# Kernel tuning notes

Measured on AMD Instinct MI355X. Metric: run time of the kernel, lower is better.

The kernel has to match this reference:

```python
import jax, jax.numpy as jnp
import numpy as np

DIM = 1024
S_SIZE = 512
M_SIZE = 4096
L_SIZE = 8192
MERGE_THRESHOLD = 0.98
L_ALPHA = 0.1
K_PROMOTE = max(1, S_SIZE // 4)  # torch: min(len(candidates), max(1, s_size//4)); candidates >> s_size here


def _l2norm(x, axis=-1):
    # F.normalize(p=2) with eps clamp
    return x / jnp.maximum(jnp.linalg.norm(x, axis=axis, keepdims=True), 1e-12)


def _update(processed_tokens, s_memory, m_memory, l_memory, m_utility, l_utility, wq, bq, wk, bk, s_ptr):
    cand = processed_tokens.reshape(-1, DIM)
    # --- S tier: scatter top-k-norm candidates into ring buffer (vectorized; K<=S so slots distinct) ---
    norms = jnp.linalg.norm(cand, axis=1)
    _, top_idx = jax.lax.top_k(norms, K_PROMOTE)
    pos = (s_ptr + jnp.arange(K_PROMOTE)) % S_SIZE
    s_mem = s_memory.at[pos].set(cand[top_idx])
    s_ptr_new = (s_ptr + K_PROMOTE) % S_SIZE
    # --- promotion attention (1 head, only attn weights used): pick best short-term slot ---
    q = l_memory.mean(axis=0) @ wq.T + bq                      # [dim]
    kproj = s_mem @ wk.T + bk                                  # [S, dim]
    attn = jax.nn.softmax(kproj @ q / jnp.sqrt(jnp.asarray(DIM, cand.dtype)))
    best_s_idx = jnp.argmax(attn)
    candidate = s_mem[best_s_idx]                              # [dim]

    # --- M tier: promote / merge / replace ---
    def not_full(mm, mu):
        ridx = jnp.argmin(mu)
        return mm.at[ridx].set(candidate), mu.at[ridx].set(mu.mean() + 1e-5)

    def full(mm, mu):
        mm_norm = _l2norm(mm)
        sims = mm_norm @ _l2norm(candidate)                    # [M]
        msi = jnp.argmax(sims)
        sim_cand = sims[msi]

        def merge_with_candidate(mm, mu):
            merged = _l2norm((mm[msi] + candidate) / 2.0)
            return mm.at[msi].set(merged), mu.at[msi].set((mu[msi] + mu.mean()) / 2.0)

        def try_internal_merge(mm, mu):
            # most redundant pair: strict lower triangle of cosine sim matrix
            sim_mat = mm_norm @ mm_norm.T                      # [M, M]
            sim_mat = jnp.where(jnp.triu(jnp.ones((M_SIZE, M_SIZE), bool)), -1.0, sim_mat)
            flat = jnp.argmax(sim_mat)
            internal_sim = sim_mat.reshape(-1)[flat]
            idx1, idx2 = flat // M_SIZE, flat % M_SIZE

            def do_pair_merge(mm, mu):
                merged = _l2norm((mm[idx1] + mm[idx2]) / 2.0)
                mm2 = mm.at[idx1].set(merged).at[idx2].set(candidate)
                mu1 = mu.at[idx1].set((mu[idx1] + mu[idx2]) / 2.0)
                mu2 = mu1.at[idx2].set(mu1.mean() + 1e-5)      # torch recomputes mean after idx1 write
                return mm2, mu2

            def replace_weakest(mm, mu):
                li = jnp.argmin(mu)
                stronger = jnp.linalg.norm(candidate) > jnp.linalg.norm(mm[li])
                mm2 = jnp.where(stronger, mm.at[li].set(candidate), mm)
                mu2 = jnp.where(stronger, mu.at[li].set(mu.mean() + 1e-5), mu)
                return mm2, mu2

            return jax.lax.cond(internal_sim > MERGE_THRESHOLD, do_pair_merge, replace_weakest, mm, mu)

        return jax.lax.cond(sim_cand > MERGE_THRESHOLD, merge_with_candidate, try_internal_merge, mm, mu)

    is_m_full = ~jnp.any(m_utility == 0)
    m_mem, m_util = jax.lax.cond(is_m_full, full, not_full, m_memory, m_utility)
    # --- L tier: consolidate most-used M slot into least-used L slot ---
    mi = jnp.argmax(m_util)
    lj = jnp.argmin(l_utility)
    consolidated = (1.0 - L_ALPHA) * l_memory[lj] + L_ALPHA * m_mem[mi]
    l_mem = l_memory.at[lj].set(consolidated)
    l_util = l_utility.at[lj].set(l_utility.mean())            # mean of pre-write values
    return s_mem, m_mem, l_mem, m_util, l_util, s_ptr_new


def setup_inputs() -> dict:
    key = jax.random.key(0)
    ks = jax.random.split(key, 10)
    scale = 1.0 / np.sqrt(DIM)
    return {
        "processed_tokens": jax.random.normal(ks[0], (4, 4096, DIM), jnp.float32),
        "s_memory": jax.random.normal(ks[1], (S_SIZE, DIM), jnp.float32),
        "m_memory": jax.random.normal(ks[2], (M_SIZE, DIM), jnp.float32),
        "l_memory": jax.random.normal(ks[3], (L_SIZE, DIM), jnp.float32),
        "m_utility": jax.random.uniform(ks[4], (M_SIZE,), jnp.float32) + 0.01,  # >0 -> 'm full' branch
        "l_utility": jax.random.uniform(ks[5], (L_SIZE,), jnp.float32) + 0.01,
        "wq": jax.random.normal(ks[6], (DIM, DIM), jnp.float32) * scale,
        "bq": jnp.zeros((DIM,), jnp.float32),
        "wk": jax.random.normal(ks[7], (DIM, DIM), jnp.float32) * scale,
        "bk": jnp.zeros((DIM,), jnp.float32),
        "s_ptr": 0,
    }


def reference(processed_tokens, s_memory, m_memory, l_memory, m_utility, l_utility, wq, bq, wk, bk, s_ptr):
    return _update(processed_tokens, s_memory, m_memory, l_memory, m_utility, l_utility, wq, bq, wk, bk, s_ptr)
```

## Files before the change

### kernel.cpp

```cpp
#include <hip/hip_runtime.h>

#define DIMV 1024
#define SSZ 512
#define MSZ 4096
#define LSZ 8192
#define KPROM 128
#define NCAND 16384
#define NPAIR 1056

typedef __attribute__((ext_vector_type(4))) float f32x4;
typedef __attribute__((ext_vector_type(4))) unsigned int u32x4;
typedef __attribute__((ext_vector_type(4))) unsigned short u16x4;
typedef __attribute__((ext_vector_type(8))) __bf16 bf16x8;

#define OUT_S 0ull
#define OUT_M 524288ull
#define OUT_L 4718592ull
#define OUT_MU 13107200ull
#define OUT_LU 13111296ull
#define OUT_SPTR 13119488ull

#define SC_BF16 0ull
#define SC_NORMS 2100000ull
#define SC_TOPIDX 2117000ull
#define SC_LPART 2120000ull
#define SC_RV 2260000ull
#define SC_LMEAN 2262000ull
#define SC_Q 2264000ull
#define SC_LOGITS 2413000ull
#define SC_BEST 2414000ull
#define SC_MNORM 2415000ull
#define SC_SIMS 2420000ull
#define SC_PPV 2425000ull
#define SC_PPI 2427000ull

__device__ __forceinline__ float wave_sum(float v) {
#pragma unroll
  for (int o = 32; o > 0; o >>= 1) v += __shfl_down(v, o, 64);
  return v;
}
__device__ __forceinline__ void wave_maxidx(float& v, int& i) {
#pragma unroll
  for (int o = 32; o > 0; o >>= 1) {
    float ov = __shfl_down(v, o, 64);
    int oi = __shfl_down(i, o, 64);
    if (ov > v || (ov == v && oi < i)) { v = ov; i = oi; }
  }
}
__device__ __forceinline__ void wave_minidx(float& v, int& i) {
#pragma unroll
  for (int o = 32; o > 0; o >>= 1) {
    float ov = __shfl_down(v, o, 64);
    int oi = __shfl_down(i, o, 64);
    if (ov < v || (ov == v && oi < i)) { v = ov; i = oi; }
  }
}
__device__ __forceinline__ unsigned short f2bf(float x) {
  unsigned u = __float_as_uint(x);
  return (unsigned short)((u + 0x7FFFu + ((u >> 16) & 1u)) >> 16);
}

__global__ void kA(const float* __restrict__ cand, const float* __restrict__ l_memory,
                   const float* __restrict__ m, float* __restrict__ norms,
                   float* __restrict__ lpart, unsigned short* __restrict__ mb,
                   float* __restrict__ mnorm) {
  int b = blockIdx.x, t = threadIdx.x, lane = t & 63, w = t >> 6;
  if (b < 4096) {
    int row = b * 4 + w;
    const f32x4* p = (const f32x4*)(cand + (size_t)row * DIMV);
    float s = 0.f;
#pragma unroll
    for (int c = 0; c < 4; ++c) {
      f32x4 v = p[c * 64 + lane];
      s += v.x * v.x + v.y * v.y + v.z * v.z + v.w * v.w;
    }
    s = wave_sum(s);
    if (lane == 0) norms[row] = sqrtf(s);
  } else if (b < 4224) {
    int bb = b - 4096;
    f32x4 a = {0.f, 0.f, 0.f, 0.f};
    const f32x4* base = (const f32x4*)(l_memory + (size_t)bb * 64 * DIMV);
    for (int r = 0; r < 64; ++r) a += base[r * 256 + t];
    ((f32x4*)(lpart + (size_t)bb * DIMV))[t] = a;
  } else {
    int row = (b - 4224) * 4 + w;
    const f32x4* mp = (const f32x4*)(m + (size_t)row * DIMV);
    float ss = 0.f;
#pragma unroll
    for (int c = 0; c < 4; ++c) {
      int i = c * 64 + lane;
      f32x4 v = mp[i];
      ss += v.x * v.x + v.y * v.y + v.z * v.z + v.w * v.w;
      u16x4 h;
      h.x = f2bf(v.x); h.y = f2bf(v.y); h.z = f2bf(v.z); h.w = f2bf(v.w);
      ((u16x4*)(mb + (size_t)row * DIMV))[i] = h;
    }
    ss = wave_sum(ss);
    if (lane == 0) mnorm[row] = sqrtf(ss);
  }
}

__device__ int scan_excl_1024(int v, int* sh, int* total) {
  int t = threadIdx.x;
  sh[t] = v;
  __syncthreads();
  for (int o = 1; o < 1024; o <<= 1) {
    int x = (t >= o) ? sh[t - o] : 0;
    __syncthreads();
    sh[t] += x;
    __syncthreads();
  }
  int incl = sh[t];
  *total = sh[1023];
  __syncthreads();
  return incl - v;
}

__global__ void kT(const float* __restrict__ norms, int* __restrict__ topidx,
                   const float* __restrict__ lpart, float* __restrict__ lmean) {
  int t = threadIdx.x;
  if (blockIdx.x == 1) {
    float s = 0.f;
    for (int p = 0; p < 128; ++p) s += lpart[(size_t)p * DIMV + t];
    lmean[t] = s * (1.f / 8192.f);
    return;
  }
  __shared__ int sh[1024];
  __shared__ int hist[256];
  __shared__ unsigned s_selkey[KPROM];
  __shared__ int s_selidx[KPROM];
  __shared__ int s_digit, s_sub;
  unsigned key[16];
#pragma unroll
  for (int j = 0; j < 16; ++j) key[j] = __float_as_uint(norms[t * 16 + j]);

  unsigned prefix = 0, himask = 0;
  int remaining = KPROM;
  for (int p = 24; p >= 0; p -= 8) {
    if (t < 256) hist[t] = 0;
    __syncthreads();
#pragma unroll
    for (int j = 0; j < 16; ++j)
      if ((key[j] & himask) == prefix) atomicAdd(&hist[(key[j] >> p) & 255], 1);
    __syncthreads();
    if (t < 256) sh[t] = hist[t];
    __syncthreads();
    for (int o = 1; o < 256; o <<= 1) {
      int x = (t < 256 && t + o < 256) ? sh[t + o] : 0;
      __syncthreads();
      if (t < 256) sh[t] += x;
      __syncthreads();
    }
    if (t < 256) {
      int sfex = (t < 255) ? sh[t + 1] : 0;
      if (sfex < remaining && remaining <= sh[t]) { s_digit = t; s_sub = sfex; }
    }
    __syncthreads();
    prefix |= ((unsigned)s_digit) << p;
    remaining -= s_sub;
    himask |= (0xFFu << p);
    __syncthreads();
  }
  unsigned T = prefix;

  int cgt = 0, ceq = 0;
#pragma unroll
  for (int j = 0; j < 16; ++j) { cgt += (key[j] > T); ceq += (key[j] == T); }
  int total_gt, total_eq;
  int sgt = scan_excl_1024(cgt, sh, &total_gt);
  int seq = scan_excl_1024(ceq, sh, &total_eq);
  int need_eq = KPROM - total_gt;
  int g = sgt, e = seq;
#pragma unroll
  for (int j = 0; j < 16; ++j) {
    if (key[j] > T) { s_selkey[g] = key[j]; s_selidx[g] = t * 16 + j; ++g; }
    else if (key[j] == T) {
      if (e < need_eq) { s_selkey[total_gt + e] = key[j]; s_selidx[total_gt + e] = t * 16 + j; }
      ++e;
    }
  }
  __syncthreads();
  if (t < KPROM) {
    unsigned mk = s_selkey[t];
    int mi = s_selidx[t];
    int rank = 0;
    for (int q2 = 0; q2 < KPROM; ++q2) {
      unsigned qk = s_selkey[q2];
      int qi = s_selidx[q2];
      rank += (qk > mk || (qk == mk && qi < mi)) ? 1 : 0;
    }
    topidx[rank] = mi;
  }
}

__global__ void kB(const float* __restrict__ cand, const float* __restrict__ s_memory,
                   const int* __restrict__ topidx, const int* __restrict__ s_ptr,
                   const float* __restrict__ wq, const float* __restrict__ bq,
                   const float* __restrict__ lmean, float* __restrict__ out_s,
                   float* __restrict__ out_sptr, float* __restrict__ qv) {
  int b = blockIdx.x, t = threadIdx.x;
  if (b < 512) {
    int sp = s_ptr[0];
    int k = (b - sp + SSZ) & (SSZ - 1);
    const float* src = (k < KPROM) ? (cand + (size_t)topidx[k] * DIMV) : (s_memory + (size_t)b * DIMV);
    ((f32x4*)(out_s + (size_t)b * DIMV))[t] = ((const f32x4*)src)[t];
    if (b == 0 && t == 0) out_sptr[0] = (float)((sp + KPROM) % SSZ);
  } else {
    int lane = t & 63, w = t >> 6;
    int d = (b - 512) * 4 + w;
    const f32x4* row = (const f32x4*)(wq + (size_t)d * DIMV);
    const f32x4* lm = (const f32x4*)lmean;
    float s = 0.f;
#pragma unroll
    for (int c = 0; c < 4; ++c) {
      f32x4 a = row[c * 64 + lane], bb = lm[c * 64 + lane];
      s += a.x * bb.x + a.y * bb.y + a.z * bb.z + a.w * bb.w;
    }
    s = wave_sum(s);
    if (lane == 0) qv[d] = s + bq[d];
  }
}

__global__ void kC(const float* __restrict__ wk, const float* __restrict__ qv,
                   float* __restrict__ rv) {
  int b = blockIdx.x, t = threadIdx.x;
  f32x4 a = {0.f, 0.f, 0.f, 0.f};
  for (int r = 0; r < 8; ++r) {
    float qd = qv[b * 8 + r];
    f32x4 v = ((const f32x4*)(wk + (size_t)(b * 8 + r) * DIMV))[t];
    a += v * qd;
  }
  atomicAdd(&rv[t * 4 + 0], a.x);
  atomicAdd(&rv[t * 4 + 1], a.y);
  atomicAdd(&rv[t * 4 + 2], a.z);
  atomicAdd(&rv[t * 4 + 3], a.w);
}

__global__ void kD(const float* __restrict__ out_s, const float* __restrict__ rv,
                   float* __restrict__ logits) {
  int lane = threadIdx.x & 63, w = threadIdx.x >> 6;
  int srow = blockIdx.x * 4 + w;
  const f32x4* a = (const f32x4*)(out_s + (size_t)srow * DIMV);
  const f32x4* b = (const f32x4*)rv;
  float s = 0.f;
#pragma unroll
  for (int c = 0; c < 4; ++c) {
    f32x4 x = a[c * 64 + lane], y = b[c * 64 + lane];
    s += x.x * y.x + x.y * y.y + x.z * y.z + x.w * y.w;
  }
  s = wave_sum(s);
  if (lane == 0) logits[srow] = s;
}

__global__ void kE(const float* __restrict__ logits, const float* __restrict__ out_s,
                   int* __restrict__ best, float* __restrict__ cnorm) {
  __shared__ float swv[4];
  __shared__ int swi[4];
  int t = threadIdx.x, lane = t & 63, w = t >> 6;
  float v0 = logits[t], v1 = logits[t + 256];
  float bv;
  int bidx;
  if (v1 > v0) { bv = v1; bidx = t + 256; } else { bv = v0; bidx = t; }
  wave_maxidx(bv, bidx);
  if (lane == 0) { swv[w] = bv; swi[w] = bidx; }
  __syncthreads();
  if (t == 0) {
    float a = swv[0]; int ai = swi[0];
    for (int i = 1; i < 4; ++i)
      if (swv[i] > a || (swv[i] == a && swi[i] < ai)) { a = swv[i]; ai = swi[i]; }
    best[0] = ai;
  }
  __syncthreads();
  int bi = best[0];
  f32x4 c4 = ((const f32x4*)(out_s + (size_t)bi * DIMV))[t];
  float s = c4.x * c4.x + c4.y * c4.y + c4.z * c4.z + c4.w * c4.w;
  s = wave_sum(s);
  __syncthreads();
  if (lane == 0) swv[w] = s;
  __syncthreads();
  if (t == 0) cnorm[0] = sqrtf(swv[0] + swv[1] + swv[2] + swv[3]);
}

__global__ __launch_bounds__(256, 4) void kG(const unsigned short* __restrict__ mb,
                                             const float* __restrict__ mnorm,
                                             const float* __restrict__ m,
                                             const float* __restrict__ out_s,
                                             const int* __restrict__ best,
                                             const float* __restrict__ cnorm,
                                             float* __restrict__ pv, int* __restrict__ pidx,
                                             float* __restrict__ sims) {
  int b = blockIdx.x, t = threadIdx.x, lane = t & 63, w = t >> 6;
  if (b >= NPAIR) {
    int row = (b - NPAIR) * 4 + w;
    const f32x4* mp = (const f32x4*)(m + (size_t)row * DIMV);
    const f32x4* cp = (const f32x4*)(out_s + (size_t)best[0] * DIMV);
    float sd = 0.f;
#pragma unroll
    for (int c = 0; c < 4; ++c) {
      int i = c * 64 + lane;
      f32x4 v = mp[i], u = cp[i];
      sd += v.x * u.x + v.y * u.y + v.z * u.z + v.w * u.w;
    }
    sd = wave_sum(sd);
    if (lane == 0) sims[row] = sd / (fmaxf(mnorm[row], 1e-12f) * fmaxf(cnorm[0], 1e-12f));
    return;
  }
  __shared__ unsigned short At[128 * 72];
  __shared__ unsigned short Bt[64 * 72];
  __shared__ float spv[4];
  __shared__ int spi[4];
  int bi = (int)((sqrtf(4.f * (float)b + 1.f) - 1.f) * 0.5f);
  while (bi * bi + bi > b) --bi;
  while ((bi + 1) * (bi + 1) + (bi + 1) <= b) ++bi;
  int bj = b - (bi * bi + bi);
  int wr = w >> 1, wc = w & 1;
  int rl = lane & 15, kq = (lane >> 4) * 8, riq = (lane >> 4) * 4;
  int rowA0 = bi * 128, rowB0 = bj * 64;

  f32x4 acc[4][2];
  f32x4 z = {0.f, 0.f, 0.f, 0.f};
#pragma unroll
  for (int i = 0; i < 4; ++i) { acc[i][0] = z; acc[i][1] = z; }

  for (int kc = 0; kc < DIMV; kc += 64) {
    __syncthreads();
#pragma unroll
    for (int c = 0; c < 6; ++c) {
      int chunk = c * 256 + t;
      if (chunk < 1024) {
        int r = chunk >> 3, g = chunk & 7;
        u32x4 va = *(const u32x4*)(mb + (size_t)(rowA0 + r) * DIMV + kc + g * 8);
        *(u32x4*)(At + r * 72 + g * 8) = va;
      } else {
        int c3 = chunk - 1024;
        int r = c3 >> 3, g = c3 & 7;
        u32x4 vb = *(const u32x4*)(mb + (size_t)(rowB0 + r) * DIMV + kc + g * 8);
        *(u32x4*)(Bt + r * 72 + g * 8) = vb;
      }
    }
    __syncthreads();
#pragma unroll
    for (int ks = 0; ks < 64; ks += 32) {
      bf16x8 af[4], bfv[2];
#pragma unroll
      for (int ti = 0; ti < 4; ++ti)
        af[ti] = *(const bf16x8*)(At + (wr * 64 + ti * 16 + rl) * 72 + ks + kq);
#pragma unroll
      for (int tj = 0; tj < 2; ++tj)
        bfv[tj] = *(const bf16x8*)(Bt + (wc * 32 + tj * 16 + rl) * 72 + ks + kq);
#pragma unroll
      for (int ti = 0; ti < 4; ++ti)
#pragma unroll
        for (int tj = 0; tj < 2; ++tj)
          acc[ti][tj] = __builtin_amdgcn_mfma_f32_16x16x32_bf16(af[ti], bfv[tj], acc[ti][tj], 0, 0, 0);
    }
  }
  float ni[16], nj[2];
#pragma unroll
  for (int ti = 0; ti < 4; ++ti)
#pragma unroll
    for (int r = 0; r < 4; ++r)
      ni[ti * 4 + r] = fmaxf(mnorm[rowA0 + wr * 64 + ti * 16 + riq + r], 1e-12f);
#pragma unroll
  for (int tj = 0; tj < 2; ++tj)
    nj[tj] = fmaxf(mnorm[rowB0 + wc * 32 + tj * 16 + rl], 1e-12f);

  float bv = -3.402823466e38f;
  int bidx = 0x7FFFFFFF;
#pragma unroll
  for (int ti = 0; ti < 4; ++ti)
#pragma unroll
    for (int tj = 0; tj < 2; ++tj)
#pragma unroll
      for (int r = 0; r < 4; ++r) {
        int gi = rowA0 + wr * 64 + ti * 16 + riq + r;
        int gj = rowB0 + wc * 32 + tj * 16 + rl;
        if (gi > gj) {
          float s = acc[ti][tj][r] / (ni[ti * 4 + r] * nj[tj]);
          int fi = gi * MSZ + gj;
          if (s > bv || (s == bv && fi < bidx)) { bv = s; bidx = fi; }
        }
      }
  wave_maxidx(bv, bidx);
  if (lane == 0) { spv[w] = bv; spi[w] = bidx; }
  __syncthreads();
  if (t == 0) {
    float a = spv[0]; int ai = spi[0];
    for (int i = 1; i < 4; ++i)
      if (spv[i] > a || (spv[i] == a && spi[i] < ai)) { a = spv[i]; ai = spi[i]; }
    pv[b] = a;
    pidx[b] = ai;
  }
}

__global__ void kH(const float* __restrict__ pv, const int* __restrict__ pidx,
                   const float* __restrict__ sims, const float* __restrict__ mu,
                   const float* __restrict__ mnorm, const float* __restrict__ cnorm,
                   const int* __restrict__ best, const float* __restrict__ lu,
                   float* __restrict__ out_mu, float* __restrict__ out_lu,
                   int* __restrict__ ws) {
  __shared__ float swv[16];
  __shared__ int swi[16];
  __shared__ float ssum[16];
  __shared__ int szf[16];
  __shared__ float s_res[2];
  __shared__ int s_resi[2];
  __shared__ int s_branch, s_i1, s_i2, s_lj;
  __shared__ float s_u1, s_u2, s_lmean;
  int t = threadIdx.x, lane = t & 63, w = t >> 6;

  float bv = -3.402823466e38f;
  int bidx = 0x7FFFFFFF;
  for (int i = t; i < NPAIR; i += 1024) {
    float v = pv[i];
    int fi = pidx[i];
    if (v > bv || (v == bv && fi < bidx)) { bv = v; bidx = fi; }
  }
  wave_maxidx(bv, bidx);
  if (lane == 0) { swv[w] = bv; swi[w] = bidx; }
  __syncthreads();
  if (t == 0) {
    float a = swv[0]; int ai = swi[0];
    for (int i = 1; i < 16; ++i)
      if (swv[i] > a || (swv[i] == a && swi[i] < ai)) { a = swv[i]; ai = swi[i]; }
    s_res[0] = a; s_resi[0] = ai;
  }
  __syncthreads();

  bv = -3.402823466e38f;
  bidx = 0x7FFFFFFF;
#pragma unroll
  for (int j = 0; j < 4; ++j) {
    int i = t * 4 + j;
    float v = sims[i];
    if (v > bv) { bv = v; bidx = i; }
  }
  wave_maxidx(bv, bidx);
  if (lane == 0) { swv[w] = bv; swi[w] = bidx; }
  __syncthreads();
  if (t == 0) {
    float a = swv[0]; int ai = swi[0];
    for (int i = 1; i < 16; ++i)
      if (swv[i] > a || (swv[i] == a && swi[i] < ai)) { a = swv[i]; ai = swi[i]; }
    s_res[1] = a; s_resi[1] = ai;
  }
  __syncthreads();

  float muv[4];
  float sum = 0.f, mnv = 3.402823466e38f;
  int mni = 0x7FFFFFFF, zf = 0;
#pragma unroll
  for (int j = 0; j < 4; ++j) {
    int i = t * 4 + j;
    float v = mu[i];
    muv[j] = v;
    sum += v;
    if (v < mnv) { mnv = v; mni = i; }
    if (v == 0.f) zf = 1;
  }
  sum = wave_sum(sum);
  wave_minidx(mnv, mni);
#pragma unroll
  for (int o = 32; o > 0; o >>= 1) zf |= __shfl_down(zf, o, 64);
  if (lane == 0) { ssum[w] = sum; swv[w] = mnv; swi[w] = mni; szf[w] = zf; }
  __syncthreads();
  if (t == 0) {
    float muSum = 0.f;
    int anyz = 0;
    float a = swv[0]; int li = swi[0];
    for (int i = 0; i < 16; ++i) {
      muSum += ssum[i];
      anyz |= szf[i];
      if (i > 0 && (swv[i] < a || (swv[i] == a && swi[i] < li))) { a = swv[i]; li = swi[i]; }
    }
    float muMean = muSum / 4096.f;
    float internal_sim = s_res[0];
    int iflat = s_resi[0];
    float sim_cand = s_res[1];
    int msi = s_resi[1];
    int branch, i1 = -1, i2 = -1;
    float u1 = 0.f, u2 = 0.f;
    if (anyz) {
      branch = 0; i1 = li; u1 = muMean + 1e-5f;
    } else if (sim_cand > 0.98f) {
      branch = 1; i1 = msi; u1 = (mu[msi] + muMean) * 0.5f;
    } else if (internal_sim > 0.98f) {
      branch = 2; i1 = iflat / MSZ; i2 = iflat - (iflat / MSZ) * MSZ;
      float o1 = mu[i1], o2 = mu[i2];
      u1 = (o1 + o2) * 0.5f;
      u2 = (muSum - o1 + u1) / 4096.f + 1e-5f;
    } else {
      if (cnorm[0] > mnorm[li]) { branch = 0; i1 = li; u1 = muMean + 1e-5f; }
      else branch = 4;
    }
    s_branch = branch; s_i1 = i1; s_i2 = i2; s_u1 = u1; s_u2 = u2;
    ws[2] = branch; ws[3] = i1; ws[4] = i2; ws[5] = best[0];
  }
  __syncthreads();

  int branch = s_branch, i1 = s_i1, i2 = s_i2;
  float u1 = s_u1, u2 = s_u2;
  bv = -3.402823466e38f;
  bidx = 0x7FFFFFFF;
#pragma unroll
  for (int j = 0; j < 4; ++j) {
    int i = t * 4 + j;
    float v = muv[j];
    if (branch != 4 && i == i1) v = u1;
    if (branch == 2 && i == i2) v = u2;
    out_mu[i] = v;
    if (v > bv) { bv = v; bidx = i; }
  }
  wave_maxidx(bv, bidx);
  __syncthreads();
  if (lane == 0) { swv[w] = bv; swi[w] = bidx; }
  __syncthreads();
  if (t == 0) {
    float a = swv[0]; int ai = swi[0];
    for (int i = 1; i < 16; ++i)
      if (swv[i] > a || (swv[i] == a && swi[i] < ai)) { a = swv[i]; ai = swi[i]; }
    ws[1] = ai;
  }

  float luv[8];
  sum = 0.f; mnv = 3.402823466e38f; mni = 0x7FFFFFFF;
#pragma unroll
  for (int j = 0; j < 8; ++j) {
    int i = t * 8 + j;
    float v = lu[i];
    luv[j] = v;
    sum += v;
    if (v < mnv) { mnv = v; mni = i; }
  }
  sum = wave_sum(sum);
  wave_minidx(mnv, mni);
  __syncthreads();
  if (lane == 0) { swv[w] = mnv; swi[w] = mni; ssum[w] = sum; }
  __syncthreads();
  if (t == 0) {
    float a = swv[0]; int ai = swi[0];
    float ls = 0.f;
    for (int i = 0; i < 16; ++i) {
      ls += ssum[i];
      if (i > 0 && (swv[i] < a || (swv[i] == a && swi[i] < ai))) { a = swv[i]; ai = swi[i]; }
    }
    s_lj = ai;
    s_lmean = ls / 8192.f;
    ws[0] = ai;
  }
  __syncthreads();
  int lj = s_lj;
  float lmv = s_lmean;
#pragma unroll
  for (int j = 0; j < 8; ++j) {
    int i = t * 8 + j;
    out_lu[i] = (i == lj) ? lmv : luv[j];
  }
}

__global__ void kI(const float* __restrict__ m, const float* __restrict__ l_memory,
                   const float* __restrict__ out_s, const int* __restrict__ ws,
                   float* __restrict__ out_m, float* __restrict__ out_l) {
  __shared__ float sred[4];
  int b = blockIdx.x, t = threadIdx.x, lane = t & 63, w = t >> 6;
  int lj = ws[0], mi = ws[1], branch = ws[2], i1 = ws[3], i2 = ws[4], best = ws[5];
  if (b < 4096) {
    int row = b;
    int mode = 0;
    if ((branch == 0 && row == i1) || (branch == 2 && row == i2)) mode = 1;
    else if (branch == 1 && row == i1) mode = 2;
    else if (branch == 2 && row == i1) mode = 3;
    f32x4* dst = (f32x4*)(out_m + (size_t)row * DIMV);
    if (mode == 0) {
      dst[t] = ((const f32x4*)(m + (size_t)row * DIMV))[t];
    } else if (mode == 1) {
      dst[t] = ((const f32x4*)(out_s + (size_t)best * DIMV))[t];
    } else {
      f32x4 a = ((const f32x4*)(m + (size_t)row * DIMV))[t];
      f32x4 bb = (mode == 2) ? ((const f32x4*)(out_s + (size_t)best * DIMV))[t]
                             : ((const f32x4*)(m + (size_t)i2 * DIMV))[t];
      f32x4 v = (a + bb) * 0.5f;
      float ss = v.x * v.x + v.y * v.y + v.z * v.z + v.w * v.w;
      ss = wave_sum(ss);
      if (lane == 0) sred[w] = ss;
      __syncthreads();
      float nrm = fmaxf(sqrtf(sred[0] + sred[1] + sred[2] + sred[3]), 1e-12f);
      dst[t] = v / nrm;
    }
  } else {
    int row = b - 4096;
    f32x4 v = ((const f32x4*)(l_memory + (size_t)row * DIMV))[t];
    if (row == lj) {
      int mode = 0;
      if ((branch == 0 && mi == i1) || (branch == 2 && mi == i2)) mode = 1;
      else if (branch == 1 && mi == i1) mode = 2;
      else if (branch == 2 && mi == i1) mode = 3;
      f32x4 mv;
      if (mode == 0) {
        mv = ((const f32x4*)(m + (size_t)mi * DIMV))[t];
      } else if (mode == 1) {
        mv = ((const f32x4*)(out_s + (size_t)best * DIMV))[t];
      } else {
        f32x4 a = ((const f32x4*)(m + (size_t)mi * DIMV))[t];
        f32x4 bb = (mode == 2) ? ((const f32x4*)(out_s + (size_t)best * DIMV))[t]
                               : ((const f32x4*)(m + (size_t)i2 * DIMV))[t];
        f32x4 vm = (a + bb) * 0.5f;
        float ss = vm.x * vm.x + vm.y * vm.y + vm.z * vm.z + vm.w * vm.w;
        ss = wave_sum(ss);
        if (lane == 0) sred[w] = ss;
        __syncthreads();
        float nrm = fmaxf(sqrtf(sred[0] + sred[1] + sred[2] + sred[3]), 1e-12f);
        mv = vm / nrm;
      }
      v = v * 0.9f + mv * 0.1f;
    }
    ((f32x4*)(out_l + (size_t)row * DIMV))[t] = v;
  }
}

extern "C" void kernel_launch(void* const* d_in, const int* in_sizes, int n_in,
                              void* d_out, int out_size, void* d_ws, size_t ws_size,
                              hipStream_t stream) {
  const float* cand = (const float*)d_in[0];
  const float* s_memory = (const float*)d_in[1];
  const float* m_memory = (const float*)d_in[2];
  const float* l_memory = (const float*)d_in[3];
  const float* m_utility = (const float*)d_in[4];
  const float* l_utility = (const float*)d_in[5];
  const float* wq = (const float*)d_in[6];
  const float* bq = (const float*)d_in[7];
  const float* wk = (const float*)d_in[8];
  const float* bk = (const float*)d_in[9];
  const int* s_ptr = (const int*)d_in[10];
  (void)bk;

  float* out = (float*)d_out;
  float* out_s = out + OUT_S;
  float* out_m = out + OUT_M;
  float* out_l = out + OUT_L;
  float* out_mu = out + OUT_MU;
  float* out_lu = out + OUT_LU;
  float* out_sptr = out + OUT_SPTR;

  float* lsc = out_l;
  unsigned short* mb = (unsigned short*)(lsc + SC_BF16);
  float* norms = lsc + SC_NORMS;
  int* topidx = (int*)(lsc + SC_TOPIDX);
  float* lpart = lsc + SC_LPART;
  float* rv = lsc + SC_RV;
  float* lmean = lsc + SC_LMEAN;
  float* qv = lsc + SC_Q;
  float* logits = lsc + SC_LOGITS;
  int* best = (int*)(lsc + SC_BEST);
  float* cnorm = lsc + SC_BEST + 1;
  float* mnorm = lsc + SC_MNORM;
  float* sims = lsc + SC_SIMS;
  float* pv = lsc + SC_PPV;
  int* pidx = (int*)(lsc + SC_PPI);
  int* wsctl = (int*)d_ws;

  hipMemsetAsync(rv, 0, 4096, stream);
  kA<<<5248, 256, 0, stream>>>(cand, l_memory, m_memory, norms, lpart, mb, mnorm);
  kT<<<2, 1024, 0, stream>>>(norms, topidx, lpart, lmean);
  kB<<<768, 256, 0, stream>>>(cand, s_memory, topidx, s_ptr, wq, bq, lmean, out_s, out_sptr, qv);
  kC<<<128, 256, 0, stream>>>(wk, qv, rv);
  kD<<<128, 256, 0, stream>>>(out_s, rv, logits);
  kE<<<1, 256, 0, stream>>>(logits, out_s, best, cnorm);
  kG<<<NPAIR + 1024, 256, 0, stream>>>(mb, mnorm, m_memory, out_s, best, cnorm, pv, pidx, sims);
  kH<<<1, 1024, 0, stream>>>(pv, pidx, sims, m_utility, mnorm, cnorm, best, l_utility,
                             out_mu, out_lu, wsctl);
  kI<<<12288, 256, 0, stream>>>(m_memory, l_memory, out_s, wsctl, out_m, out_l);
}
```

Measured before the change: 323.9 us.

## Use 128x128 triangular tiles with direct-to-LDS loads and XOR swizzle in pair-sim GEMM

The M×M cosine-similarity kernel now uses square 128x128 lower-triangle tiles instead of 128x64, which halves the number of pair blocks and raises arithmetic intensity per tile. Tile loads go through global_load_lds (direct to LDS) into an XOR-swizzled layout instead of padded register staging. The block index is interleaved so neighbouring blocks spread across the triangle. The cost is more accumulator registers, so launch bounds drop to 3 blocks per SM, and fewer blocks may underfill the GPU.

```diff
diff --git a/kernel.cpp b/kernel.cpp
--- a/kernel.cpp
+++ b/kernel.cpp
@@ -6,7 +6,7 @@
 #define LSZ 8192
 #define KPROM 128
 #define NCAND 16384
-#define NPAIR 1056
+#define NPAIR 528
 
 typedef __attribute__((ext_vector_type(4))) float f32x4;
 typedef __attribute__((ext_vector_type(4))) unsigned int u32x4;
@@ -58,6 +58,10 @@
 __device__ __forceinline__ unsigned short f2bf(float x) {
   unsigned u = __float_as_uint(x);
   return (unsigned short)((u + 0x7FFFu + ((u >> 16) & 1u)) >> 16);
+}
+__device__ __forceinline__ void gload16(const unsigned short* g, unsigned short* l) {
+  __builtin_amdgcn_global_load_lds((const __attribute__((address_space(1))) unsigned int*)(g),
+                                   (__attribute__((address_space(3))) unsigned int*)(l), 16, 0, 0);
 }
 
 __global__ void kA(const float* __restrict__ cand, const float* __restrict__ l_memory,
@@ -281,7 +285,7 @@
   if (t == 0) cnorm[0] = sqrtf(swv[0] + swv[1] + swv[2] + swv[3]);
 }
 
-__global__ __launch_bounds__(256, 4) void kG(const unsigned short* __restrict__ mb,
+__global__ __launch_bounds__(256, 3) void kG(const unsigned short* __restrict__ mb,
                                              const float* __restrict__ mnorm,
                                              const float* __restrict__ m,
                                              const float* __restrict__ out_s,
@@ -305,78 +309,80 @@
     if (lane == 0) sims[row] = sd / (fmaxf(mnorm[row], 1e-12f) * fmaxf(cnorm[0], 1e-12f));
     return;
   }
-  __shared__ unsigned short At[128 * 72];
-  __shared__ unsigned short Bt[64 * 72];
+  __shared__ unsigned short Ash[128 * 64];
+  __shared__ unsigned short Bsh[128 * 64];
   __shared__ float spv[4];
   __shared__ int spi[4];
-  int bi = (int)((sqrtf(4.f * (float)b + 1.f) - 1.f) * 0.5f);
-  while (bi * bi + bi > b) --bi;
-  while ((bi + 1) * (bi + 1) + (bi + 1) <= b) ++bi;
-  int bj = b - (bi * bi + bi);
+
+  int bs = (b & 7) * 66 + (b >> 3);
+  int bi = (int)((sqrtf(8.f * (float)bs + 1.f) - 1.f) * 0.5f);
+  while (bi * (bi + 1) / 2 > bs) --bi;
+  while ((bi + 1) * (bi + 2) / 2 <= bs) ++bi;
+  int bj = bs - bi * (bi + 1) / 2;
+  int rowA0 = bi * 128, rowB0 = bj * 128;
+
   int wr = w >> 1, wc = w & 1;
-  int rl = lane & 15, kq = (lane >> 4) * 8, riq = (lane >> 4) * 4;
-  int rowA0 = bi * 128, rowB0 = bj * 64;
-
-  f32x4 acc[4][2];
+  int rl = lane & 15, kq4 = lane >> 4;
+  int swz = rl & 7;
+  int subrow = lane >> 3, gg = lane & 7;
+  int gsw = (gg ^ subrow) << 3;
+
+  f32x4 acc[4][4];
   f32x4 z = {0.f, 0.f, 0.f, 0.f};
 #pragma unroll
-  for (int i = 0; i < 4; ++i) { acc[i][0] = z; acc[i][1] = z; }
+  for (int ti = 0; ti < 4; ++ti)
+#pragma unroll
+    for (int tj = 0; tj < 4; ++tj) acc[ti][tj] = z;
 
   for (int kc = 0; kc < DIMV; kc += 64) {
-    __syncthreads();
-#pragma unroll
-    for (int c = 0; c < 6; ++c) {
-      int chunk = c * 256 + t;
-      if (chunk < 1024) {
-        int r = chunk >> 3, g = chunk & 7;
-        u32x4 va = *(const u32x4*)(mb + (size_t)(rowA0 + r) * DIMV + kc + g * 8);
-        *(u32x4*)(At + r * 72 + g * 8) = va;
-      } else {
-        int c3 = chunk - 1024;
-        int r = c3 >> 3, g = c3 & 7;
-        u32x4 vb = *(const u32x4*)(mb + (size_t)(rowB0 + r) * DIMV + kc + g * 8);
-        *(u32x4*)(Bt + r * 72 + g * 8) = vb;
-      }
-    }
-    __syncthreads();
-#pragma unroll
-    for (int ks = 0; ks < 64; ks += 32) {
-      bf16x8 af[4], bfv[2];
+#pragma unroll
+    for (int jj = 0; jj < 4; ++jj) {
+      int rsub = w * 32 + jj * 8 + subrow;
+      gload16(mb + (size_t)(rowA0 + rsub) * DIMV + kc + gsw, Ash + (w * 4 + jj) * 512);
+      gload16(mb + (size_t)(rowB0 + rsub) * DIMV + kc + gsw, Bsh + (w * 4 + jj) * 512);
+    }
+    __syncthreads();
+#pragma unroll
+    for (int ks = 0; ks < 2; ++ks) {
+      int co = (((ks * 4 + kq4) ^ swz) << 3);
+      bf16x8 af[4], bfv[4];
 #pragma unroll
       for (int ti = 0; ti < 4; ++ti)
-        af[ti] = *(const bf16x8*)(At + (wr * 64 + ti * 16 + rl) * 72 + ks + kq);
-#pragma unroll
-      for (int tj = 0; tj < 2; ++tj)
-        bfv[tj] = *(const bf16x8*)(Bt + (wc * 32 + tj * 16 + rl) * 72 + ks + kq);
+        af[ti] = *(const bf16x8*)(Ash + (wr * 64 + ti * 16 + rl) * 64 + co);
+#pragma unroll
+      for (int tj = 0; tj < 4; ++tj)
+        bfv[tj] = *(const bf16x8*)(Bsh + (wc * 64 + tj * 16 + rl) * 64 + co);
 #pragma unroll
       for (int ti = 0; ti < 4; ++ti)
 #pragma unroll
-        for (int tj = 0; tj < 2; ++tj)
+        for (int tj = 0; tj < 4; ++tj)
           acc[ti][tj] = __builtin_amdgcn_mfma_f32_16x16x32_bf16(af[ti], bfv[tj], acc[ti][tj], 0, 0, 0);
     }
-  }
-  float ni[16], nj[2];
+    __syncthreads();
+  }
+
+  float ni[16], nj4[4];
 #pragma unroll
   for (int ti = 0; ti < 4; ++ti)
 #pragma unroll
     for (int r = 0; r < 4; ++r)
-      ni[ti * 4 + r] = fmaxf(mnorm[rowA0 + wr * 64 + ti * 16 + riq + r], 1e-12f);
-#pragma unroll
-  for (int tj = 0; tj < 2; ++tj)
-    nj[tj] = fmaxf(mnorm[rowB0 + wc * 32 + tj * 16 + rl], 1e-12f);
+      ni[ti * 4 + r] = fmaxf(mnorm[rowA0 + wr * 64 + ti * 16 + kq4 * 4 + r], 1e-12f);
+#pragma unroll
+  for (int tj = 0; tj < 4; ++tj)
+    nj4[tj] = fmaxf(mnorm[rowB0 + wc * 64 + tj * 16 + rl], 1e-12f);
 
   float bv = -3.402823466e38f;
   int bidx = 0x7FFFFFFF;
 #pragma unroll
   for (int ti = 0; ti < 4; ++ti)
 #pragma unroll
-    for (int tj = 0; tj < 2; ++tj)
+    for (int tj = 0; tj < 4; ++tj)
 #pragma unroll
       for (int r = 0; r < 4; ++r) {
-        int gi = rowA0 + wr * 64 + ti * 16 + riq + r;
-        int gj = rowB0 + wc * 32 + tj * 16 + rl;
+        int gi = rowA0 + wr * 64 + ti * 16 + kq4 * 4 + r;
+        int gj = rowB0 + wc * 64 + tj * 16 + rl;
         if (gi > gj) {
-          float s = acc[ti][tj][r] / (ni[ti * 4 + r] * nj[tj]);
+          float s = acc[ti][tj][r] / (ni[ti * 4 + r] * nj4[tj]);
           int fi = gi * MSZ + gj;
           if (s > bv || (s == bv && fi < bidx)) { bv = s; bidx = fi; }
         }
```

After: 289.2 us. 10.7% less time.
